# Optimization experiments

Hardware: AMD Instinct MI355X
Metric: run time of the kernel (lower is better)

Reference implementation:

```python
import jax, jax.numpy as jnp
import numpy as np

DN = ('NCHW', 'OIHW', 'NCHW')

def _conv(x, w, b, pad):
    y = jax.lax.conv_general_dilated(x, w, (1, 1), pad, dimension_numbers=DN)
    return y + b[None, :, None, None]

def setup_inputs() -> dict:
    key = jax.random.key(0)
    ks = jax.random.split(key, 8)
    B, C, H, W = 8, 256, 64, 64
    C8 = C // 8
    return {
        'x': jax.random.normal(ks[0], (B, C, H, W), jnp.float32),
        'wq': jax.random.normal(ks[1], (C8, C, 1, 3), jnp.float32) * 0.02,
        'bq': jax.random.normal(ks[2], (C8,), jnp.float32) * 0.02,
        'wk': jax.random.normal(ks[3], (C8, C, 3, 1), jnp.float32) * 0.02,
        'bk': jax.random.normal(ks[4], (C8,), jnp.float32) * 0.02,
        'wv': jax.random.normal(ks[5], (C, C, 1, 1), jnp.float32) * 0.02,
        'bv': jax.random.normal(ks[6], (C,), jnp.float32) * 0.02,
        'gamma': jax.random.normal(ks[7], (1,), jnp.float32),
    }

def reference(x, wq, bq, wk, bk, wv, bv, gamma):
    B, C, H, W = x.shape
    N = H * W
    # q: (1,3) kernel, pad (0,1); k: (3,1) kernel, pad (1,0); v: 1x1
    q = _conv(x, wq, bq, [(0, 0), (1, 1)]).reshape(B, -1, N)  # B, C/8, N
    k = _conv(x, wk, bk, [(1, 1), (0, 0)]).reshape(B, -1, N)  # B, C/8, N
    v = _conv(x, wv, bv, [(0, 0), (0, 0)]).reshape(B, C, N)   # B, C, N
    affinity = jnp.einsum('bci,bcj->bij', q, k)               # B, N, N
    affinity = jax.nn.softmax(affinity, axis=-1)
    # weights = v @ affinity^T  ->  (B, C, N)
    weights = jnp.einsum('bcj,bij->bci', v, affinity).reshape(B, C, H, W)
    return gamma[0] * weights + x
```

## Files before the change

kernel.cpp:

```cpp
#include <hip/hip_runtime.h>
#include <math.h>

#define BB 8
#define CCH 256
#define C8 32
#define NN 4096
#define LOG2E 1.44269504f

typedef unsigned short us;
typedef __attribute__((ext_vector_type(8))) short bf16x8;
typedef __attribute__((ext_vector_type(4))) float f32x4;
typedef __attribute__((ext_vector_type(16))) float f32x16;

static __device__ __forceinline__ us f2bf(float f) {
  union { float f; unsigned u; } v; v.f = f;
  unsigned r = v.u + 0x7fffu + ((v.u >> 16) & 1u);
  return (us)(r >> 16);
}
static __device__ __forceinline__ us f2bf_rhu(float f) {
  return (us)((__float_as_uint(f) + 0x8000u) >> 16);
}
template <int CTRL>
static __device__ __forceinline__ float dpp_mv(float x) {
  return __int_as_float(
      __builtin_amdgcn_update_dpp(0, __float_as_int(x), CTRL, 0xF, 0xF, false));
}
static __device__ __forceinline__ float rowsum16(float t) {
  t += dpp_mv<0x121>(t);
  t += dpp_mv<0x122>(t);
  t += dpp_mv<0x124>(t);
  t += dpp_mv<0x128>(t);
  return t;
}

__global__ __launch_bounds__(256) void prep_kernel(
    const float* __restrict__ x, const float* __restrict__ wq,
    const float* __restrict__ wk, const float* __restrict__ wv,
    us* __restrict__ xT, us* __restrict__ wqc, us* __restrict__ wkc,
    us* __restrict__ wvb) {
  __shared__ __align__(16) us lt[64 * 68];
  int bid = blockIdx.x;
  int tid = threadIdx.x;
  if (bid < 2048) {
    int b = bid >> 8, cb = (bid >> 6) & 3, nb = bid & 63;
    const float* xb = x + (((size_t)(b * 256 + cb * 64)) << 12);
    int nl = tid & 63, ch = tid >> 6;
#pragma unroll
    for (int p = 0; p < 16; p++) {
      int c = p * 4 + ch;
      lt[nl * 68 + c] = f2bf(xb[((size_t)c << 12) + (nb * 64 + nl)]);
    }
    __syncthreads();
    us* xTb = xT + (((size_t)b << 12) + nb * 64) * 256 + cb * 64;
    int cw = tid & 7, nr0 = tid >> 3;
#pragma unroll
    for (int p2 = 0; p2 < 2; p2++) {
      int nr = p2 * 32 + nr0;
      uint2 lo = *(const uint2*)&lt[nr * 68 + cw * 8];
      uint2 hi = *(const uint2*)&lt[nr * 68 + cw * 8 + 4];
      *(uint4*)&xTb[(size_t)nr * 256 + cw * 8] = make_uint4(lo.x, lo.y, hi.x, hi.y);
    }
  } else {
    int idx = (bid - 2048) * 256 + tid;
    if (idx < 24576) {
      int oc = idx / 768, r = idx % 768, t = r >> 8, ic = r & 255;
      wqc[idx] = f2bf(wq[(oc * 256 + ic) * 3 + t] * LOG2E);
    } else if (idx < 49152) {
      int j = idx - 24576;
      int oc = j / 768, r = j % 768, t = r >> 8, ic = r & 255;
      wkc[j] = f2bf(wk[(oc * 256 + ic) * 3 + t]);
    } else if (idx < 114688) {
      int j = idx - 49152;
      wvb[j] = f2bf(wv[j]);
    }
  }
}

__global__ __launch_bounds__(256) void conv_kernel(
    const us* __restrict__ xT, const us* __restrict__ wqc,
    const us* __restrict__ wkc, const float* __restrict__ bq,
    const float* __restrict__ bk, const us* __restrict__ wvb,
    const float* __restrict__ bv, us* __restrict__ qT, us* __restrict__ kT,
    us* __restrict__ vblk) {
  int tid = threadIdx.x, lane = tid & 63, w = tid >> 6;
  int l15 = lane & 15, quad = lane >> 4;
  if (blockIdx.x < 512) {
    int bid = blockIdx.x;
    int b = bid & 7, rt = bid >> 3;
    int n0 = rt * 64, y = rt;
    bool isq = (w < 2);
    int m0 = (w & 1) * 16;
    const us* wc = isq ? wqc : wkc;
    const us* xTb = xT + (((size_t)b << 12) * 256);
    f32x4 acc[4];
#pragma unroll
    for (int nt = 0; nt < 4; nt++) acc[nt] = (f32x4){0.f, 0.f, 0.f, 0.f};
#pragma unroll
    for (int t = 0; t < 3; t++) {
      bool killT = (!isq) && ((t == 0 && y == 0) || (t == 2 && y == 63));
      if (!killT) {
        int dn = isq ? (t - 1) : (t - 1) * 64;
#pragma unroll
        for (int k8 = 0; k8 < 8; k8++) {
          int kloc = t * 256 + k8 * 32 + quad * 8;
          bf16x8 af = *(const bf16x8*)(wc + (size_t)(m0 + l15) * 768 + kloc);
          int ic = k8 * 32 + quad * 8;
#pragma unroll
          for (int nt = 0; nt < 4; nt++) {
            int nl = nt * 16 + l15;
            int ns = n0 + nl + dn;
            ns = ns < 0 ? 0 : (ns > 4095 ? 4095 : ns);
            bf16x8 bf = *(const bf16x8*)(xTb + (size_t)ns * 256 + ic);
            if (isq && ((t == 0 && nl == 0) || (t == 2 && nl == 63)))
              bf = (bf16x8){0, 0, 0, 0, 0, 0, 0, 0};
            acc[nt] = __builtin_amdgcn_mfma_f32_16x16x32_bf16(af, bf, acc[nt], 0, 0, 0);
          }
        }
      }
    }
    const float* bias = isq ? bq : bk;
    float bsc = isq ? LOG2E : 1.0f;
    us* outp = (isq ? qT : kT) + (((size_t)b << 12) * 32);
    float b0 = bias[m0 + quad * 4 + 0] * bsc;
    float b1 = bias[m0 + quad * 4 + 1] * bsc;
    float b2 = bias[m0 + quad * 4 + 2] * bsc;
    float b3 = bias[m0 + quad * 4 + 3] * bsc;
#pragma unroll
    for (int nt = 0; nt < 4; nt++) {
      int n = n0 + nt * 16 + l15;
      unsigned lo = (unsigned)f2bf(acc[nt][0] + b0) | ((unsigned)f2bf(acc[nt][1] + b1) << 16);
      unsigned hi = (unsigned)f2bf(acc[nt][2] + b2) | ((unsigned)f2bf(acc[nt][3] + b3) << 16);
      *(uint2*)(outp + (size_t)n * 32 + m0 + quad * 4) = make_uint2(lo, hi);
    }
  } else {
    int bid = blockIdx.x - 512;
    int b = bid & 7, nt0 = bid >> 3;
    int n0 = nt0 * 64;
    const us* xTb = xT + (((size_t)b << 12) * 256);
    f32x4 acc[4][4];
#pragma unroll
    for (int ct = 0; ct < 4; ct++)
#pragma unroll
      for (int nt = 0; nt < 4; nt++) acc[ct][nt] = (f32x4){0.f, 0.f, 0.f, 0.f};
#pragma unroll
    for (int kk = 0; kk < 8; kk++) {
      bf16x8 bfr[4];
#pragma unroll
      for (int nt = 0; nt < 4; nt++)
        bfr[nt] = *(const bf16x8*)(xTb + (size_t)(n0 + nt * 16 + l15) * 256 + kk * 32 + quad * 8);
#pragma unroll
      for (int ct = 0; ct < 4; ct++) {
        bf16x8 af = *(const bf16x8*)(wvb + (size_t)(w * 64 + ct * 16 + l15) * 256 + kk * 32 + quad * 8);
#pragma unroll
        for (int nt = 0; nt < 4; nt++)
          acc[ct][nt] = __builtin_amdgcn_mfma_f32_16x16x32_bf16(af, bfr[nt], acc[ct][nt], 0, 0, 0);
      }
    }
    us* vb = vblk + ((size_t)b << 20);
#pragma unroll
    for (int ct = 0; ct < 4; ct++) {
#pragma unroll
      for (int r = 0; r < 4; r++) {
        int oc = w * 64 + ct * 16 + quad * 4 + r;
        float bvv = bv[oc];
#pragma unroll
        for (int nt = 0; nt < 4; nt++) {
          vb[((size_t)((n0 >> 4) + nt) * 256 + oc) * 16 + l15] = f2bf(acc[ct][nt][r] + bvv);
        }
      }
    }
  }
}

__global__ __launch_bounds__(512, 4) void attn_kernel(
    const float* __restrict__ x, const us* __restrict__ qT,
    const us* __restrict__ kT, const us* __restrict__ vblk,
    const float* __restrict__ gamma_p, float* __restrict__ out) {
  __shared__ __align__(16) us pb[2][64 * 72];
  __shared__ float lpart[2][64];

  int tid = threadIdx.x, lane = tid & 63, w = tid >> 6;
  int l15 = lane & 15, quad = lane >> 4;
  int l31 = lane & 31, h32 = lane >> 5;
  int tw = w & 3, jh = w >> 2;

  int bid = blockIdx.x;
  int b = bid & 7, i0 = (bid >> 3) * 64;

  const us* qTb = qT + (((size_t)b << 12) * 32);
  const us* kTb = kT + (((size_t)b << 12) * 32);
  const us* vbb = vblk + ((size_t)b << 20);

  bf16x8 qf = *(const bf16x8*)(qTb + (size_t)(i0 + tw * 16 + l15) * 32 + quad * 8);

  float lr[4] = {0.f, 0.f, 0.f, 0.f};
  f32x16 o[2];
#pragma unroll
  for (int it = 0; it < 2; it++)
#pragma unroll
    for (int rg = 0; rg < 16; rg++) o[it][rg] = 0.f;

  int bu = 0;
  for (int jt = 0; jt < 64; jt++) {
    int j0 = jt * 64;
    bf16x8 kf0 = *(const bf16x8*)(kTb + (size_t)(j0 + jh * 32 + l15) * 32 + quad * 8);
    bf16x8 kf1 = *(const bf16x8*)(kTb + (size_t)(j0 + jh * 32 + 16 + l15) * 32 + quad * 8);
    bf16x8 vf[4];
#pragma unroll
    for (int ks = 0; ks < 4; ks++)
      vf[ks] = *(const bf16x8*)(vbb + ((size_t)((j0 >> 4) + ks) * 256 + w * 32 + l31) * 16 + h32 * 8);
    f32x4 s0 = __builtin_amdgcn_mfma_f32_16x16x32_bf16(qf, kf0, (f32x4){0.f, 0.f, 0.f, 0.f}, 0, 0, 0);
    f32x4 s1 = __builtin_amdgcn_mfma_f32_16x16x32_bf16(qf, kf1, (f32x4){0.f, 0.f, 0.f, 0.f}, 0, 0, 0);
    us* pw = &pb[bu][(tw * 16 + quad * 4) * 72 + jh * 32 + l15];
#pragma unroll
    for (int r = 0; r < 4; r++) {
      float p0 = __builtin_amdgcn_exp2f(s0[r]);
      float p1 = __builtin_amdgcn_exp2f(s1[r]);
      lr[r] += p0 + p1;
      pw[r * 72] = f2bf_rhu(p0);
      pw[r * 72 + 16] = f2bf_rhu(p1);
    }
    __syncthreads();
#pragma unroll
    for (int ks = 0; ks < 4; ks++) {
      bf16x8 pf0 = *(const bf16x8*)&pb[bu][(size_t)l31 * 72 + ks * 16 + h32 * 8];
      bf16x8 pf1 = *(const bf16x8*)&pb[bu][(size_t)(32 + l31) * 72 + ks * 16 + h32 * 8];
      o[0] = __builtin_amdgcn_mfma_f32_32x32x16_bf16(vf[ks], pf0, o[0], 0, 0, 0);
      o[1] = __builtin_amdgcn_mfma_f32_32x32x16_bf16(vf[ks], pf1, o[1], 0, 0, 0);
    }
    bu ^= 1;
  }

  float ls[4];
#pragma unroll
  for (int r = 0; r < 4; r++) ls[r] = rowsum16(lr[r]);
  if (l15 == 0) {
#pragma unroll
    for (int r = 0; r < 4; r++) lpart[jh][tw * 16 + quad * 4 + r] = ls[r];
  }
  __syncthreads();
  float g = gamma_p[0];
  const float* xb = x + ((size_t)b << 20);
  float* ob = out + ((size_t)b << 20);
  float gl[2];
#pragma unroll
  for (int it = 0; it < 2; it++) {
    int i = it * 32 + l31;
    gl[it] = g / (lpart[0][i] + lpart[1][i]);
  }
#pragma unroll
  for (int it = 0; it < 2; it++) {
    int i = i0 + it * 32 + l31;
#pragma unroll
    for (int rg = 0; rg < 16; rg++) {
      int c = w * 32 + ((rg & 3) + 8 * (rg >> 2) + 4 * h32);
      size_t idx = ((size_t)c << 12) + i;
      ob[idx] = o[it][rg] * gl[it] + xb[idx];
    }
  }
}

extern "C" void kernel_launch(void* const* d_in, const int* in_sizes, int n_in,
                              void* d_out, int out_size, void* d_ws, size_t ws_size,
                              hipStream_t stream) {
  const float* x = (const float*)d_in[0];
  const float* wq = (const float*)d_in[1];
  const float* bq = (const float*)d_in[2];
  const float* wk = (const float*)d_in[3];
  const float* bk = (const float*)d_in[4];
  const float* wv = (const float*)d_in[5];
  const float* bv = (const float*)d_in[6];
  const float* gamma = (const float*)d_in[7];
  float* out = (float*)d_out;

  us* xT = (us*)d_ws;
  us* qT = xT + (size_t)8388608;
  us* kT = qT + (size_t)1048576;
  us* vblk = kT + (size_t)1048576;
  us* wqc = vblk + (size_t)8388608;
  us* wkc = wqc + (size_t)24576;
  us* wvb = wkc + (size_t)24576;

  prep_kernel<<<2496, 256, 0, stream>>>(x, wq, wk, wv, xT, wqc, wkc, wvb);
  conv_kernel<<<1024, 256, 0, stream>>>(xT, wqc, wkc, bq, bk, wvb, bv, qT, kT, vblk);
  attn_kernel<<<512, 512, 0, stream>>>(x, qT, kT, vblk, gamma, out);
}
```

Before: 234.0 us.

## Shrink attention query tile to 32 and software-pipeline K/V loads with setprio

The attention kernel now covers 32 query rows per block instead of 64 and launches twice as many blocks with higher occupancy bounds. It also prefetches K one tile ahead with double-buffered registers, packs exp results via v_cvt_pk_bf16_f32, raises MFMA priority with s_setprio, and uses a raw s_barrier. The aim is more parallelism and hidden load latency, at the cost of loading V twice as often overall and larger per-row reductions across four key quarters.

```diff
diff --git a/kernel.cpp b/kernel.cpp
--- a/kernel.cpp
+++ b/kernel.cpp
@@ -1,10 +1,6 @@
 #include <hip/hip_runtime.h>
 #include <math.h>
 
-#define BB 8
-#define CCH 256
-#define C8 32
-#define NN 4096
 #define LOG2E 1.44269504f
 
 typedef unsigned short us;
@@ -16,21 +12,6 @@
   union { float f; unsigned u; } v; v.f = f;
   unsigned r = v.u + 0x7fffu + ((v.u >> 16) & 1u);
   return (us)(r >> 16);
-}
-static __device__ __forceinline__ us f2bf_rhu(float f) {
-  return (us)((__float_as_uint(f) + 0x8000u) >> 16);
-}
-template <int CTRL>
-static __device__ __forceinline__ float dpp_mv(float x) {
-  return __int_as_float(
-      __builtin_amdgcn_update_dpp(0, __float_as_int(x), CTRL, 0xF, 0xF, false));
-}
-static __device__ __forceinline__ float rowsum16(float t) {
-  t += dpp_mv<0x121>(t);
-  t += dpp_mv<0x122>(t);
-  t += dpp_mv<0x124>(t);
-  t += dpp_mv<0x128>(t);
-  return t;
 }
 
 __global__ __launch_bounds__(256) void prep_kernel(
@@ -172,91 +153,114 @@
   }
 }
 
-__global__ __launch_bounds__(512, 4) void attn_kernel(
+__global__ __launch_bounds__(512, 8) void attn_kernel(
     const float* __restrict__ x, const us* __restrict__ qT,
     const us* __restrict__ kT, const us* __restrict__ vblk,
     const float* __restrict__ gamma_p, float* __restrict__ out) {
-  __shared__ __align__(16) us pb[2][64 * 72];
-  __shared__ float lpart[2][64];
+  __shared__ __align__(16) us pb[2][32 * 72];
+  __shared__ float lpart[4][32];
 
   int tid = threadIdx.x, lane = tid & 63, w = tid >> 6;
   int l15 = lane & 15, quad = lane >> 4;
   int l31 = lane & 31, h32 = lane >> 5;
-  int tw = w & 3, jh = w >> 2;
+  int iw = w & 1, jq = w >> 1;
 
   int bid = blockIdx.x;
-  int b = bid & 7, i0 = (bid >> 3) * 64;
+  int b = bid & 7, i0 = (bid >> 3) * 32;
 
   const us* qTb = qT + (((size_t)b << 12) * 32);
   const us* kTb = kT + (((size_t)b << 12) * 32);
   const us* vbb = vblk + ((size_t)b << 20);
 
-  bf16x8 qf = *(const bf16x8*)(qTb + (size_t)(i0 + tw * 16 + l15) * 32 + quad * 8);
-
-  float lr[4] = {0.f, 0.f, 0.f, 0.f};
-  f32x16 o[2];
-#pragma unroll
-  for (int it = 0; it < 2; it++)
-#pragma unroll
-    for (int rg = 0; rg < 16; rg++) o[it][rg] = 0.f;
-
-  int bu = 0;
-  for (int jt = 0; jt < 64; jt++) {
-    int j0 = jt * 64;
-    bf16x8 kf0 = *(const bf16x8*)(kTb + (size_t)(j0 + jh * 32 + l15) * 32 + quad * 8);
-    bf16x8 kf1 = *(const bf16x8*)(kTb + (size_t)(j0 + jh * 32 + 16 + l15) * 32 + quad * 8);
-    bf16x8 vf[4];
-#pragma unroll
-    for (int ks = 0; ks < 4; ks++)
-      vf[ks] = *(const bf16x8*)(vbb + ((size_t)((j0 >> 4) + ks) * 256 + w * 32 + l31) * 16 + h32 * 8);
-    f32x4 s0 = __builtin_amdgcn_mfma_f32_16x16x32_bf16(qf, kf0, (f32x4){0.f, 0.f, 0.f, 0.f}, 0, 0, 0);
-    f32x4 s1 = __builtin_amdgcn_mfma_f32_16x16x32_bf16(qf, kf1, (f32x4){0.f, 0.f, 0.f, 0.f}, 0, 0, 0);
-    us* pw = &pb[bu][(tw * 16 + quad * 4) * 72 + jh * 32 + l15];
-#pragma unroll
-    for (int r = 0; r < 4; r++) {
-      float p0 = __builtin_amdgcn_exp2f(s0[r]);
-      float p1 = __builtin_amdgcn_exp2f(s1[r]);
-      lr[r] += p0 + p1;
-      pw[r * 72] = f2bf_rhu(p0);
-      pw[r * 72 + 16] = f2bf_rhu(p1);
-    }
-    __syncthreads();
-#pragma unroll
-    for (int ks = 0; ks < 4; ks++) {
-      bf16x8 pf0 = *(const bf16x8*)&pb[bu][(size_t)l31 * 72 + ks * 16 + h32 * 8];
-      bf16x8 pf1 = *(const bf16x8*)&pb[bu][(size_t)(32 + l31) * 72 + ks * 16 + h32 * 8];
-      o[0] = __builtin_amdgcn_mfma_f32_32x32x16_bf16(vf[ks], pf0, o[0], 0, 0, 0);
-      o[1] = __builtin_amdgcn_mfma_f32_32x32x16_bf16(vf[ks], pf1, o[1], 0, 0, 0);
-    }
-    bu ^= 1;
-  }
-
-  float ls[4];
-#pragma unroll
-  for (int r = 0; r < 4; r++) ls[r] = rowsum16(lr[r]);
-  if (l15 == 0) {
-#pragma unroll
-    for (int r = 0; r < 4; r++) lpart[jh][tw * 16 + quad * 4 + r] = ls[r];
-  }
+  bf16x8 qf = *(const bf16x8*)(qTb + (size_t)(i0 + iw * 16 + l15) * 32 + quad * 8);
+
+  const us* kbase = kTb + (size_t)(jq * 16 + l15) * 32 + quad * 8;
+  const us* vbase = vbb + (size_t)(w * 32 + l31) * 16 + h32 * 8;
+  int pwi = (iw * 16 + l15) * 72 + jq * 16 + quad * 4;
+  int pri = l31 * 72 + h32 * 8;
+
+  float lr = 0.f;
+  f32x4 s;
+  f32x16 o;
+#pragma unroll
+  for (int rg = 0; rg < 16; rg++) o[rg] = 0.f;
+
+  bf16x8 kX, kY;
+  bf16x8 vf0, vf1, vf2, vf3;
+
+#define PREK(N, KD)                                                            \
+  do { KD = *(const bf16x8*)(kbase + (size_t)((N) & 63) * 2048); } while (0)
+
+#define PREV(N)                                                                \
+  do {                                                                         \
+    const us* vp = vbase + (size_t)((N) & 63) * 16384;                         \
+    vf0 = *(const bf16x8*)(vp);                                                \
+    vf1 = *(const bf16x8*)(vp + 4096);                                         \
+    vf2 = *(const bf16x8*)(vp + 8192);                                         \
+    vf3 = *(const bf16x8*)(vp + 12288);                                        \
+  } while (0)
+
+#define STEP(N, KC, KN, BUF)                                                   \
+  do {                                                                         \
+    __builtin_amdgcn_s_setprio(1);                                             \
+    s = __builtin_amdgcn_mfma_f32_16x16x32_bf16(KC, qf, (f32x4){0.f, 0.f, 0.f, 0.f}, 0, 0, 0); \
+    __builtin_amdgcn_s_setprio(0);                                             \
+    PREV(N);                                                                   \
+    PREK((N) + 1, KN);                                                         \
+    {                                                                          \
+      float p0 = __builtin_amdgcn_exp2f(s[0]);                                 \
+      float p1 = __builtin_amdgcn_exp2f(s[1]);                                 \
+      float p2 = __builtin_amdgcn_exp2f(s[2]);                                 \
+      float p3 = __builtin_amdgcn_exp2f(s[3]);                                 \
+      lr += (p0 + p1) + (p2 + p3);                                             \
+      unsigned e0, e1;                                                         \
+      asm("v_cvt_pk_bf16_f32 %0, %1, %2" : "=v"(e0) : "v"(p0), "v"(p1));       \
+      asm("v_cvt_pk_bf16_f32 %0, %1, %2" : "=v"(e1) : "v"(p2), "v"(p3));       \
+      *(uint2*)((us*)pb + (BUF) * (32 * 72) + pwi) = make_uint2(e0, e1);       \
+    }                                                                          \
+    asm volatile("s_waitcnt lgkmcnt(0)" ::: "memory");                         \
+    __builtin_amdgcn_s_barrier();                                              \
+    __builtin_amdgcn_sched_barrier(0);                                         \
+    {                                                                          \
+      const us* pr = (const us*)pb + (BUF) * (32 * 72) + pri;                  \
+      __builtin_amdgcn_s_setprio(1);                                           \
+      bf16x8 pf;                                                               \
+      pf = *(const bf16x8*)(pr + 0);                                           \
+      o = __builtin_amdgcn_mfma_f32_32x32x16_bf16(vf0, pf, o, 0, 0, 0);        \
+      pf = *(const bf16x8*)(pr + 16);                                          \
+      o = __builtin_amdgcn_mfma_f32_32x32x16_bf16(vf1, pf, o, 0, 0, 0);        \
+      pf = *(const bf16x8*)(pr + 32);                                          \
+      o = __builtin_amdgcn_mfma_f32_32x32x16_bf16(vf2, pf, o, 0, 0, 0);        \
+      pf = *(const bf16x8*)(pr + 48);                                          \
+      o = __builtin_amdgcn_mfma_f32_32x32x16_bf16(vf3, pf, o, 0, 0, 0);        \
+      __builtin_amdgcn_s_setprio(0);                                           \
+    }                                                                          \
+  } while (0)
+
+  PREK(0, kX);
+  for (int n2 = 0; n2 < 32; n2++) {
+    STEP(2 * n2, kX, kY, 0);
+    STEP(2 * n2 + 1, kY, kX, 1);
+  }
+#undef PREK
+#undef PREV
+#undef STEP
+
+  float lt = lr;
+  lt += __shfl_xor(lt, 16);
+  lt += __shfl_xor(lt, 32);
+  if (quad == 0) lpart[jq][iw * 16 + l15] = lt;
   __syncthreads();
   float g = gamma_p[0];
   const float* xb = x + ((size_t)b << 20);
   float* ob = out + ((size_t)b << 20);
-  float gl[2];
-#pragma unroll
-  for (int it = 0; it < 2; it++) {
-    int i = it * 32 + l31;
-    gl[it] = g / (lpart[0][i] + lpart[1][i]);
-  }
-#pragma unroll
-  for (int it = 0; it < 2; it++) {
-    int i = i0 + it * 32 + l31;
-#pragma unroll
-    for (int rg = 0; rg < 16; rg++) {
-      int c = w * 32 + ((rg & 3) + 8 * (rg >> 2) + 4 * h32);
-      size_t idx = ((size_t)c << 12) + i;
-      ob[idx] = o[it][rg] * gl[it] + xb[idx];
-    }
+  float gl = g / (lpart[0][l31] + lpart[1][l31] + lpart[2][l31] + lpart[3][l31]);
+  int i = i0 + l31;
+#pragma unroll
+  for (int rg = 0; rg < 16; rg++) {
+    int c = w * 32 + ((rg & 3) + 8 * (rg >> 2) + 4 * h32);
+    size_t idx = ((size_t)c << 12) + i;
+    ob[idx] = o[rg] * gl + xb[idx];
   }
 }
 
@@ -283,5 +287,5 @@
 
   prep_kernel<<<2496, 256, 0, stream>>>(x, wq, wk, wv, xT, wqc, wkc, wvb);
   conv_kernel<<<1024, 256, 0, stream>>>(xT, wqc, wkc, bq, bk, wvb, bv, qT, kT, vblk);
-  attn_kernel<<<512, 512, 0, stream>>>(x, qT, kT, vblk, gamma, out);
-}
+  attn_kernel<<<1024, 512, 0, stream>>>(x, qT, kT, vblk, gamma, out);
+}
```

After: 248.9 us. +6.4%, slower.
